# Kernel optimization log

Hardware: AMD Instinct MI355X
Metric: run time of the kernel (lower is better)

The kernel has to match this reference:

```python
import jax, jax.numpy as jnp
import numpy as np

S = 7          # number of slots
B = 8192       # batch
D = 1024       # input_dim
E = 256        # slot_embedding_dim
H = 512        # rnn_hidden_dim
SH = 256       # slot_hidden_dim
V = 100        # labels per slot (uniform)


def _lstm_cell(x, h, c, W_ih, W_hh, b_ih, b_hh):
    # PyTorch LSTMCell: gates ordered i, f, g, o
    gates = x @ W_ih.T + b_ih + h @ W_hh.T + b_hh
    i, f, g, o = jnp.split(gates, 4, axis=-1)
    i = jax.nn.sigmoid(i); f = jax.nn.sigmoid(f)
    g = jnp.tanh(g); o = jax.nn.sigmoid(o)
    c_new = f * c + i * g
    h_new = o * jnp.tanh(c_new)
    return h_new, c_new


def setup_inputs() -> dict:
    key = jax.random.key(0)
    ks = jax.random.split(key, 24)
    sc = 0.05
    D0 = D + E  # layer-0 input size
    inp = {
        'inputs': jax.random.normal(ks[0], (B, D), jnp.float32),
        'labels': jax.random.randint(ks[1], (S - 1, B), 0, V),
        'start': jax.random.normal(ks[2], (E,), jnp.float32),
        'emb': jax.random.normal(ks[3], (S - 1, V, E), jnp.float32) * sc,
        # layer 0 (input size D0)
        'W_ih0': jax.random.normal(ks[4], (S, 4 * H, D0), jnp.float32) * sc,
        'W_hh0': jax.random.normal(ks[5], (S, 4 * H, H), jnp.float32) * sc,
        'b_ih0': jax.random.normal(ks[6], (S, 4 * H), jnp.float32) * sc,
        'b_hh0': jax.random.normal(ks[7], (S, 4 * H), jnp.float32) * sc,
        'hwN_W0': jax.random.normal(ks[8], (S, H, D0 + H), jnp.float32) * sc,
        'hwN_b0': jax.random.normal(ks[9], (S, H), jnp.float32) * sc,
        'hwL_W0': jax.random.normal(ks[10], (S, H, D0), jnp.float32) * sc,
        # layer 1 (input size H)
        'W_ih1': jax.random.normal(ks[11], (S, 4 * H, H), jnp.float32) * sc,
        'W_hh1': jax.random.normal(ks[12], (S, 4 * H, H), jnp.float32) * sc,
        'b_ih1': jax.random.normal(ks[13], (S, 4 * H), jnp.float32) * sc,
        'b_hh1': jax.random.normal(ks[14], (S, 4 * H), jnp.float32) * sc,
        'hwN_W1': jax.random.normal(ks[15], (S, H, H + H), jnp.float32) * sc,
        'hwN_b1': jax.random.normal(ks[16], (S, H), jnp.float32) * sc,
        'hwL_W1': jax.random.normal(ks[17], (S, H, H), jnp.float32) * sc,
        # slot hidden + classifier
        'sh_W': jax.random.normal(ks[18], (S, SH, H), jnp.float32) * sc,
        'sh_b': jax.random.normal(ks[19], (S, SH), jnp.float32) * sc,
        'pred_W': jax.random.normal(ks[20], (S, V, SH), jnp.float32) * sc,
        'pred_b': jax.random.normal(ks[21], (S, V), jnp.float32) * sc,
    }
    return inp


def reference(inputs, labels, start, emb,
              W_ih0, W_hh0, b_ih0, b_hh0, hwN_W0, hwN_b0, hwL_W0,
              W_ih1, W_hh1, b_ih1, b_hh1, hwN_W1, hwN_b1, hwL_W1,
              sh_W, sh_b, pred_W, pred_b):
    bsz = inputs.shape[0]
    cur_emb = jnp.broadcast_to(start[None, :], (bsz, E))
    h0 = jnp.zeros((bsz, H), inputs.dtype); c0 = jnp.zeros((bsz, H), inputs.dtype)
    h1 = jnp.zeros((bsz, H), inputs.dtype); c1 = jnp.zeros((bsz, H), inputs.dtype)
    logits_all = []
    for i in range(S):  # slots are a short, structurally distinct recurrence
        x = jnp.concatenate([inputs, cur_emb], axis=-1)  # [B, D+E]
        # layer 0
        h0, c0 = _lstm_cell(x, h0, c0, W_ih0[i], W_hh0[i], b_ih0[i], b_hh0[i])
        gate = jax.nn.sigmoid(jnp.concatenate([x, h0], -1) @ hwN_W0[i].T + hwN_b0[i])
        cur = gate * h0 + (1.0 - gate) * (x @ hwL_W0[i].T)
        # layer 1
        h1, c1 = _lstm_cell(cur, h1, c1, W_ih1[i], W_hh1[i], b_ih1[i], b_hh1[i])
        gate1 = jax.nn.sigmoid(jnp.concatenate([cur, h1], -1) @ hwN_W1[i].T + hwN_b1[i])
        # (highway output of last layer feeds nothing further for this slot)
        _ = gate1 * h1 + (1.0 - gate1) * (cur @ hwL_W1[i].T)
        hidden = jax.nn.relu(h1 @ sh_W[i].T + sh_b[i])     # [B, SH]
        logits_all.append(hidden @ pred_W[i].T + pred_b[i])  # [B, V]
        if i < S - 1:
            cur_emb = emb[i][labels[i]]  # teacher-forced embedding lookup
    return jnp.stack(logits_all, axis=0)  # [S, B, V]
```

## Files before the change

kernel.cpp:

```cpp
#include <hip/hip_runtime.h>

#define SLOTS 7
#define BATCH 8192

typedef __attribute__((ext_vector_type(8))) __bf16 bf16x8;
typedef __attribute__((ext_vector_type(4))) float f32x4;

__device__ __forceinline__ void gl_lds16(const __bf16* g, __bf16* l) {
  __builtin_amdgcn_global_load_lds(
      (const __attribute__((address_space(1))) void*)g,
      (__attribute__((address_space(3))) void*)l, 16, 0, 0);
}

__device__ __forceinline__ float sigmoidf_(float x) {
  return 1.f / (1.f + __expf(-x));
}
__device__ __forceinline__ float tanhf_(float x) {
  float xc = fminf(fmaxf(x, -15.f), 15.f);
  float e = __expf(2.f * xc);
  return (e - 1.f) / (e + 1.f);
}

__global__ void __launch_bounds__(256, 4)
gemm_lstm(const __bf16* __restrict__ A, int lda,
          const __bf16* __restrict__ Bw, int ldb,
          const float* __restrict__ b_ih, const float* __restrict__ b_hh,
          float* __restrict__ cst, __bf16* __restrict__ hout, int hld, int hoff,
          int K) {
  __shared__ __align__(16) __bf16 As[2][128 * 32];
  __shared__ __align__(16) __bf16 Bs[2][128 * 32];
  const int w = threadIdx.x >> 6;
  const int lane = threadIdx.x & 63;
  const int wr = w >> 1, wc = w & 1;
  const int rowBase = blockIdx.y << 7;
  const int colBase = blockIdx.x << 7;
  const int sr = lane >> 2;
  const int scs = (((lane & 3) ^ ((sr >> 1) & 3)) << 3);

  f32x4 acc[4][4];
#pragma unroll
  for (int i = 0; i < 4; ++i)
#pragma unroll
    for (int j = 0; j < 4; ++j) acc[i][j] = (f32x4){0.f, 0.f, 0.f, 0.f};

  const int nsteps = K >> 5;

#define STAGE(bi, k0)                                                            \
  {                                                                              \
    const __bf16* ga = A + (size_t)(rowBase + (w << 5) + sr) * lda + (k0) + scs; \
    gl_lds16(ga, &As[(bi)][(w << 5) * 32]);                                      \
    gl_lds16(ga + (size_t)16 * lda, &As[(bi)][((w << 5) + 16) * 32]);            \
    const __bf16* gb = Bw + (size_t)(colBase + (w << 5) + sr) * ldb + (k0) + scs;\
    gl_lds16(gb, &Bs[(bi)][(w << 5) * 32]);                                      \
    gl_lds16(gb + (size_t)16 * ldb, &Bs[(bi)][((w << 5) + 16) * 32]);            \
  }

  STAGE(0, 0);
  __syncthreads();
  int buf = 0;
  const int ln = lane & 15;
  const int lh = lane >> 4;
  const int swz = ((lh ^ ((ln >> 1) & 3)) << 3);
  for (int t = 0; t < nsteps; ++t) {
    if (t + 1 < nsteps) STAGE(buf ^ 1, (t + 1) << 5);
    bf16x8 av[4], bv[4];
#pragma unroll
    for (int i = 0; i < 4; ++i)
      av[i] = *(const bf16x8*)&As[buf][((wr << 6) + (i << 4) + ln) * 32 + swz];
#pragma unroll
    for (int i = 0; i < 4; ++i)
      bv[i] = *(const bf16x8*)&Bs[buf][((wc << 6) + (i << 4) + ln) * 32 + swz];
#pragma unroll
    for (int mi = 0; mi < 4; ++mi)
#pragma unroll
      for (int ni = 0; ni < 4; ++ni)
        acc[mi][ni] = __builtin_amdgcn_mfma_f32_16x16x32_bf16(
            av[mi], bv[ni], acc[mi][ni], 0, 0, 0);
    __syncthreads();
    buf ^= 1;
  }
#undef STAGE

  const int row0 = rowBase + (wr << 6) + (lh << 2);
  const int h = (((colBase >> 6) + wc) << 4) + ln;
  const float bs0 = b_ih[h] + b_hh[h];
  const float bs1 = b_ih[512 + h] + b_hh[512 + h];
  const float bs2 = b_ih[1024 + h] + b_hh[1024 + h];
  const float bs3 = b_ih[1536 + h] + b_hh[1536 + h];
#pragma unroll
  for (int mi = 0; mi < 4; ++mi)
#pragma unroll
    for (int r = 0; r < 4; ++r) {
      const int row = row0 + (mi << 4) + r;
      float gi = sigmoidf_(acc[mi][0][r] + bs0);
      float gf = sigmoidf_(acc[mi][1][r] + bs1);
      float gg = tanhf_(acc[mi][2][r] + bs2);
      float go = sigmoidf_(acc[mi][3][r] + bs3);
      const size_t ci = (size_t)row * 512 + h;
      float cn = gf * cst[ci] + gi * gg;
      cst[ci] = cn;
      hout[(size_t)row * hld + hoff + h] = (__bf16)(go * tanhf_(cn));
    }
}

template <int MODE>
__global__ void __launch_bounds__(256)
gemm_bt(const __bf16* __restrict__ A, int lda,
        const __bf16* __restrict__ Bw, int ldb,
        void* __restrict__ Cout, int ldc,
        const float* __restrict__ bias,
        const float* __restrict__ auxr,
        __bf16* __restrict__ hout, int hld, int hoff,
        const __bf16* __restrict__ hsrc,
        int M, int N, int K, int Nreal) {
  __shared__ __align__(16) __bf16 As[2][128 * 32];
  __shared__ __align__(16) __bf16 Bs[2][128 * 32];
  const int w = threadIdx.x >> 6;
  const int lane = threadIdx.x & 63;
  const int wr = w >> 1, wc = w & 1;
  const int rowBase = blockIdx.y << 7;
  const int colBase = blockIdx.x << 7;
  const int sr = lane >> 2;
  const int sc = (lane & 3) << 3;

  f32x4 acc[4][4];
#pragma unroll
  for (int i = 0; i < 4; ++i)
#pragma unroll
    for (int j = 0; j < 4; ++j) acc[i][j] = (f32x4){0.f, 0.f, 0.f, 0.f};

  const int nsteps = K >> 5;

#define STAGE(bi, k0)                                                           \
  {                                                                             \
    const __bf16* ga = A + (size_t)(rowBase + (w << 5) + sr) * lda + (k0) + sc; \
    gl_lds16(ga, &As[(bi)][(w << 5) * 32]);                                     \
    gl_lds16(ga + (size_t)16 * lda, &As[(bi)][((w << 5) + 16) * 32]);           \
    const __bf16* gb = Bw + (size_t)(colBase + (w << 5) + sr) * ldb + (k0) + sc;\
    gl_lds16(gb, &Bs[(bi)][(w << 5) * 32]);                                     \
    gl_lds16(gb + (size_t)16 * ldb, &Bs[(bi)][((w << 5) + 16) * 32]);           \
  }

  STAGE(0, 0);
  __syncthreads();
  int buf = 0;
  const int ln = lane & 15;
  const int kg = (lane >> 4) << 3;
  for (int t = 0; t < nsteps; ++t) {
    if (t + 1 < nsteps) STAGE(buf ^ 1, (t + 1) << 5);
    bf16x8 av[4], bv[4];
#pragma unroll
    for (int i = 0; i < 4; ++i)
      av[i] = *(const bf16x8*)&As[buf][((wr << 6) + (i << 4) + ln) * 32 + kg];
#pragma unroll
    for (int i = 0; i < 4; ++i)
      bv[i] = *(const bf16x8*)&Bs[buf][((wc << 6) + (i << 4) + ln) * 32 + kg];
#pragma unroll
    for (int mi = 0; mi < 4; ++mi)
#pragma unroll
      for (int ni = 0; ni < 4; ++ni)
        acc[mi][ni] = __builtin_amdgcn_mfma_f32_16x16x32_bf16(
            av[mi], bv[ni], acc[mi][ni], 0, 0, 0);
    __syncthreads();
    buf ^= 1;
  }
#undef STAGE

  const int lh = lane >> 4;
  const int row0 = rowBase + (wr << 6) + (lh << 2);
  const int col0 = colBase + (wc << 6) + ln;

  if (MODE == 0) {
    float* C = (float*)Cout;
#pragma unroll
    for (int mi = 0; mi < 4; ++mi)
#pragma unroll
      for (int ni = 0; ni < 4; ++ni) {
        const int col = col0 + (ni << 4);
#pragma unroll
        for (int r = 0; r < 4; ++r)
          C[(size_t)(row0 + (mi << 4) + r) * ldc + col] = acc[mi][ni][r];
      }
  } else if (MODE == 1) {
    __bf16* C = (__bf16*)Cout;
#pragma unroll
    for (int mi = 0; mi < 4; ++mi)
#pragma unroll
      for (int ni = 0; ni < 4; ++ni) {
        const int col = col0 + (ni << 4);
        const float b = bias[col];
#pragma unroll
        for (int r = 0; r < 4; ++r) {
          float v = fmaxf(acc[mi][ni][r] + b, 0.f);
          C[(size_t)(row0 + (mi << 4) + r) * ldc + col] = (__bf16)v;
        }
      }
  } else if (MODE == 2) {
    float* C = (float*)Cout;
#pragma unroll
    for (int mi = 0; mi < 4; ++mi)
#pragma unroll
      for (int ni = 0; ni < 4; ++ni) {
        const int col = col0 + (ni << 4);
        if (col < Nreal) {
          const float b = bias[col];
#pragma unroll
          for (int r = 0; r < 4; ++r)
            C[(size_t)(row0 + (mi << 4) + r) * ldc + col] = acc[mi][ni][r] + b;
        }
      }
  } else if (MODE == 6) {
    __bf16* C = (__bf16*)Cout;
#pragma unroll
    for (int mi = 0; mi < 4; ++mi)
#pragma unroll
      for (int ni = 0; ni < 4; ++ni) {
        const int col = col0 + (ni << 4);
#pragma unroll
        for (int r = 0; r < 4; ++r) {
          const int row = row0 + (mi << 4) + r;
          float xp = auxr[(size_t)row * 1024 + col];
          float hwl = auxr[(size_t)row * 1024 + 512 + col];
          float gn = sigmoidf_(acc[mi][ni][r] + xp + bias[col]);
          float hn = (float)hsrc[(size_t)row * 512 + col];
          C[(size_t)row * ldc + col] = (__bf16)(gn * hn + (1.f - gn) * hwl);
          hout[(size_t)row * hld + hoff + col] = (__bf16)hn;
        }
      }
  }
}

#define PR0 2621440
#define PR1 3670016
#define PR2 4325376
#define PR3 4980736
#define PR4 5242880
#define PR5 6291456
#define PR6 7340032
#define PR7 7471104
#define PR8 7503872
__global__ void pack_all(const float* __restrict__ W_ih0, const float* __restrict__ W_hh0,
                         const float* __restrict__ hwN_W0, const float* __restrict__ hwL_W0,
                         const float* __restrict__ W_ih1, const float* __restrict__ W_hh1,
                         const float* __restrict__ sh_W, const float* __restrict__ pred_W,
                         __bf16* __restrict__ WA, __bf16* __restrict__ WX,
                         __bf16* __restrict__ WH, __bf16* __restrict__ WB,
                         __bf16* __restrict__ WS, __bf16* __restrict__ WP, int s) {
  const int idx = blockIdx.x * 256 + threadIdx.x;
  if (idx >= PR8) return;
  if (idx < PR0) {
    int i = idx, r = i / 1280, c = i - r * 1280;
    int sr = (((r >> 4) & 3) << 9) + ((r >> 6) << 4) + (r & 15);
    WA[(long)r * 1792 + c] = (__bf16)W_ih0[(size_t)s * 2048 * 1280 + (long)sr * 1280 + c];
  } else if (idx < PR1) {
    int i = idx - PR0, r = i >> 9, c = i & 511;
    int sr = (((r >> 4) & 3) << 9) + ((r >> 6) << 4) + (r & 15);
    WA[(long)r * 1792 + 1280 + c] = (__bf16)W_hh0[(size_t)s * 2048 * 512 + (long)sr * 512 + c];
  } else if (idx < PR2) {
    int i = idx - PR1, r = i / 1280, c = i - r * 1280;
    WX[(long)r * 1280 + c] = (__bf16)hwN_W0[(size_t)s * 512 * 1792 + (long)r * 1792 + c];
  } else if (idx < PR3) {
    int i = idx - PR2, r = i / 1280, c = i - r * 1280;
    WX[(long)(512 + r) * 1280 + c] = (__bf16)hwL_W0[(size_t)s * 512 * 1280 + (long)r * 1280 + c];
  } else if (idx < PR4) {
    int i = idx - PR3, r = i >> 9, c = i & 511;
    WH[(long)r * 512 + c] = (__bf16)hwN_W0[(size_t)s * 512 * 1792 + (long)r * 1792 + 1280 + c];
  } else if (idx < PR5) {
    int i = idx - PR4, r = i >> 9, c = i & 511;
    int sr = (((r >> 4) & 3) << 9) + ((r >> 6) << 4) + (r & 15);
    WB[(long)r * 1024 + c] = (__bf16)W_ih1[(size_t)s * 2048 * 512 + (long)sr * 512 + c];
  } else if (idx < PR6) {
    int i = idx - PR5, r = i >> 9, c = i & 511;
    int sr = (((r >> 4) & 3) << 9) + ((r >> 6) << 4) + (r & 15);
    WB[(long)r * 1024 + 512 + c] = (__bf16)W_hh1[(size_t)s * 2048 * 512 + (long)sr * 512 + c];
  } else if (idx < PR7) {
    int i = idx - PR6, r = i >> 9, c = i & 511;
    WS[(long)r * 512 + c] = (__bf16)sh_W[(size_t)s * 256 * 512 + (long)r * 512 + c];
  } else {
    int i = idx - PR7, r = i >> 8, c = i & 255;
    float v = (r < 100) ? pred_W[(size_t)s * 100 * 256 + (long)r * 256 + c] : 0.f;
    WP[(long)r * 256 + c] = (__bf16)v;
  }
}

__global__ void conv_inputs(const float* __restrict__ in, __bf16* __restrict__ xh) {
  int idx = blockIdx.x * 256 + threadIdx.x;
  int b = idx >> 10, c = idx & 1023;
  xh[(size_t)b * 1792 + c] = (__bf16)in[idx];
}

__global__ void set_start(const float* __restrict__ start, __bf16* __restrict__ xh) {
  int idx = blockIdx.x * 256 + threadIdx.x;
  int b = idx >> 8, e = idx & 255;
  xh[(size_t)b * 1792 + 1024 + e] = (__bf16)start[e];
}

__global__ void emb_gather(const float* __restrict__ emb, const int* __restrict__ labels,
                           __bf16* __restrict__ xh) {
  int idx = blockIdx.x * 256 + threadIdx.x;
  int b = idx >> 8, e = idx & 255;
  int lab = labels[b];
  xh[(size_t)b * 1792 + 1024 + e] = (__bf16)emb[(size_t)lab * 256 + e];
}

__global__ void zero_states(__bf16* __restrict__ xh, __bf16* __restrict__ xh1A) {
  int idx = blockIdx.x * 256 + threadIdx.x;
  int b = idx >> 9, h = idx & 511;
  xh[(size_t)b * 1792 + 1280 + h] = (__bf16)0.f;
  xh1A[(size_t)b * 1024 + 512 + h] = (__bf16)0.f;
}

extern "C" void kernel_launch(void* const* d_in, const int* in_sizes, int n_in,
                              void* d_out, int out_size, void* d_ws, size_t ws_size,
                              hipStream_t stream) {
  const float* inputs = (const float*)d_in[0];
  const int* labels = (const int*)d_in[1];
  const float* start = (const float*)d_in[2];
  const float* emb = (const float*)d_in[3];
  const float* W_ih0 = (const float*)d_in[4];
  const float* W_hh0 = (const float*)d_in[5];
  const float* b_ih0 = (const float*)d_in[6];
  const float* b_hh0 = (const float*)d_in[7];
  const float* hwN_W0 = (const float*)d_in[8];
  const float* hwN_b0 = (const float*)d_in[9];
  const float* hwL_W0 = (const float*)d_in[10];
  const float* W_ih1 = (const float*)d_in[11];
  const float* W_hh1 = (const float*)d_in[12];
  const float* b_ih1 = (const float*)d_in[13];
  const float* b_hh1 = (const float*)d_in[14];
  const float* sh_W = (const float*)d_in[18];
  const float* sh_b = (const float*)d_in[19];
  const float* pred_W = (const float*)d_in[20];
  const float* pred_b = (const float*)d_in[21];
  float* out = (float*)d_out;

  char* p = (char*)d_ws;
  size_t off = 0;
  auto alloc = [&](size_t bytes) {
    void* r = p + off;
    off += (bytes + 255) & ~(size_t)255;
    return r;
  };
  __bf16* WA = (__bf16*)alloc((size_t)2048 * 1792 * 2);
  __bf16* WX = (__bf16*)alloc((size_t)1024 * 1280 * 2);
  __bf16* WH = (__bf16*)alloc((size_t)512 * 512 * 2);
  __bf16* WB = (__bf16*)alloc((size_t)2048 * 1024 * 2);
  __bf16* WS = (__bf16*)alloc((size_t)256 * 512 * 2);
  __bf16* WP = (__bf16*)alloc((size_t)128 * 256 * 2);
  __bf16* xh = (__bf16*)alloc((size_t)BATCH * 1792 * 2);
  __bf16* xh1A = (__bf16*)alloc((size_t)BATCH * 1024 * 2);
  __bf16* xh1B = (__bf16*)alloc((size_t)BATCH * 1024 * 2);
  __bf16* h0new = (__bf16*)alloc((size_t)BATCH * 512 * 2);
  float* ghw = (float*)alloc((size_t)BATCH * 1024 * 4);
  float* c0 = (float*)alloc((size_t)BATCH * 512 * 4);
  float* c1 = (float*)alloc((size_t)BATCH * 512 * 4);
  __bf16* hidden = (__bf16*)ghw;
  (void)ws_size; (void)in_sizes; (void)n_in; (void)out_size;

  hipMemsetAsync(c0, 0, (size_t)BATCH * 512 * 4, stream);
  hipMemsetAsync(c1, 0, (size_t)BATCH * 512 * 4, stream);
  zero_states<<<BATCH * 512 / 256, 256, 0, stream>>>(xh, xh1A);
  conv_inputs<<<BATCH * 1024 / 256, 256, 0, stream>>>(inputs, xh);
  set_start<<<BATCH * 256 / 256, 256, 0, stream>>>(start, xh);

  const dim3 blk(256);
  for (int s = 0; s < SLOTS; ++s) {
    __bf16* xcur = (s & 1) ? xh1B : xh1A;
    __bf16* xnext = (s & 1) ? xh1A : xh1B;
    pack_all<<<(PR8 + 255) / 256, blk, 0, stream>>>(
        W_ih0, W_hh0, hwN_W0, hwL_W0, W_ih1, W_hh1, sh_W, pred_W,
        WA, WX, WH, WB, WS, WP, s);

    gemm_bt<0><<<dim3(8, 64), blk, 0, stream>>>(
        xh, 1792, WX, 1280, ghw, 1024, nullptr,
        nullptr, nullptr, 0, 0, nullptr, BATCH, 1024, 1280, 1024);
    gemm_lstm<<<dim3(16, 64), blk, 0, stream>>>(
        xh, 1792, WA, 1792, b_ih0 + s * 2048, b_hh0 + s * 2048,
        c0, h0new, 512, 0, 1792);
    gemm_bt<6><<<dim3(4, 64), blk, 0, stream>>>(
        h0new, 512, WH, 512, xcur, 1024, hwN_b0 + s * 512,
        ghw, xh, 1792, 1280, h0new, BATCH, 512, 512, 512);
    if (s < SLOTS - 1)
      emb_gather<<<BATCH * 256 / 256, blk, 0, stream>>>(
          emb + (size_t)s * 100 * 256, labels + (size_t)s * BATCH, xh);
    gemm_lstm<<<dim3(16, 64), blk, 0, stream>>>(
        xcur, 1024, WB, 1024, b_ih1 + s * 2048, b_hh1 + s * 2048,
        c1, xnext, 1024, 512, 1024);
    gemm_bt<1><<<dim3(2, 64), blk, 0, stream>>>(
        xnext + 512, 1024, WS, 512, hidden, 256, sh_b + s * 256,
        nullptr, nullptr, 0, 0, nullptr, BATCH, 256, 512, 256);
    gemm_bt<2><<<dim3(1, 64), blk, 0, stream>>>(
        hidden, 256, WP, 256, out + (size_t)s * BATCH * 100, 100,
        pred_b + s * 100, nullptr, nullptr, 0, 0, nullptr, BATCH, 128, 256, 100);
  }
}
```

Measured before the change: 1.695 ms.

## Remap blocks across XCDs, store highway preactivations in bf16, fuse embedding gather

Adds an XCD-aware block index remap to both GEMM kernels so consecutive tiles land on the same chiplet, which should improve L2 reuse. The intermediate buffer holding x-projections for the highway gate and linear path is stored in bf16 instead of fp32, halving its write and read traffic. The per-slot embedding gather kernel is removed and folded into the MODE 6 highway epilogue, saving a launch. The bf16 intermediate adds rounding error to the gate and linear terms, and the remap assumes the block count is divisible by 8.

New measurement: 1.584 ms. -6.6%, faster.

```diff
diff --git a/kernel.cpp b/kernel.cpp
--- a/kernel.cpp
+++ b/kernel.cpp
@@ -19,6 +19,15 @@
   float xc = fminf(fmaxf(x, -15.f), 15.f);
   float e = __expf(2.f * xc);
   return (e - 1.f) / (e + 1.f);
+}
+
+__device__ __forceinline__ void xcd_remap(int& bx, int& by) {
+  const int NBx = gridDim.x;
+  const int NB = NBx * gridDim.y;
+  int id = by * NBx + bx;
+  id = (id & 7) * (NB >> 3) + (id >> 3);
+  bx = id % NBx;
+  by = id / NBx;
 }
 
 __global__ void __launch_bounds__(256, 4)
@@ -32,8 +41,10 @@
   const int w = threadIdx.x >> 6;
   const int lane = threadIdx.x & 63;
   const int wr = w >> 1, wc = w & 1;
-  const int rowBase = blockIdx.y << 7;
-  const int colBase = blockIdx.x << 7;
+  int bx = blockIdx.x, by = blockIdx.y;
+  xcd_remap(bx, by);
+  const int rowBase = by << 7;
+  const int colBase = bx << 7;
   const int sr = lane >> 2;
   const int scs = (((lane & 3) ^ ((sr >> 1) & 3)) << 3);
 
@@ -109,17 +120,20 @@
         const __bf16* __restrict__ Bw, int ldb,
         void* __restrict__ Cout, int ldc,
         const float* __restrict__ bias,
-        const float* __restrict__ auxr,
+        const __bf16* __restrict__ auxr,
         __bf16* __restrict__ hout, int hld, int hoff,
         const __bf16* __restrict__ hsrc,
+        const float* __restrict__ embp, const int* __restrict__ labels, int do_emb,
         int M, int N, int K, int Nreal) {
   __shared__ __align__(16) __bf16 As[2][128 * 32];
   __shared__ __align__(16) __bf16 Bs[2][128 * 32];
   const int w = threadIdx.x >> 6;
   const int lane = threadIdx.x & 63;
   const int wr = w >> 1, wc = w & 1;
-  const int rowBase = blockIdx.y << 7;
-  const int colBase = blockIdx.x << 7;
+  int bx = blockIdx.x, by = blockIdx.y;
+  xcd_remap(bx, by);
+  const int rowBase = by << 7;
+  const int colBase = bx << 7;
   const int sr = lane >> 2;
   const int sc = (lane & 3) << 3;
 
@@ -170,18 +184,7 @@
   const int row0 = rowBase + (wr << 6) + (lh << 2);
   const int col0 = colBase + (wc << 6) + ln;
 
-  if (MODE == 0) {
-    float* C = (float*)Cout;
-#pragma unroll
-    for (int mi = 0; mi < 4; ++mi)
-#pragma unroll
-      for (int ni = 0; ni < 4; ++ni) {
-        const int col = col0 + (ni << 4);
-#pragma unroll
-        for (int r = 0; r < 4; ++r)
-          C[(size_t)(row0 + (mi << 4) + r) * ldc + col] = acc[mi][ni][r];
-      }
-  } else if (MODE == 1) {
+  if (MODE == 1) {
     __bf16* C = (__bf16*)Cout;
 #pragma unroll
     for (int mi = 0; mi < 4; ++mi)
@@ -209,6 +212,17 @@
             C[(size_t)(row0 + (mi << 4) + r) * ldc + col] = acc[mi][ni][r] + b;
         }
       }
+  } else if (MODE == 7) {
+    __bf16* C = (__bf16*)Cout;
+#pragma unroll
+    for (int mi = 0; mi < 4; ++mi)
+#pragma unroll
+      for (int ni = 0; ni < 4; ++ni) {
+        const int col = col0 + (ni << 4);
+#pragma unroll
+        for (int r = 0; r < 4; ++r)
+          C[(size_t)(row0 + (mi << 4) + r) * ldc + col] = (__bf16)acc[mi][ni][r];
+      }
   } else if (MODE == 6) {
     __bf16* C = (__bf16*)Cout;
 #pragma unroll
@@ -219,14 +233,29 @@
 #pragma unroll
         for (int r = 0; r < 4; ++r) {
           const int row = row0 + (mi << 4) + r;
-          float xp = auxr[(size_t)row * 1024 + col];
-          float hwl = auxr[(size_t)row * 1024 + 512 + col];
+          float xp = (float)auxr[(size_t)row * 1024 + col];
+          float hwl = (float)auxr[(size_t)row * 1024 + 512 + col];
           float gn = sigmoidf_(acc[mi][ni][r] + xp + bias[col]);
           float hn = (float)hsrc[(size_t)row * 512 + col];
           C[(size_t)row * ldc + col] = (__bf16)(gn * hn + (1.f - gn) * hwl);
           hout[(size_t)row * hld + hoff + col] = (__bf16)hn;
         }
       }
+    if (do_emb && colBase < 256) {
+#pragma unroll
+      for (int mi = 0; mi < 4; ++mi)
+#pragma unroll
+        for (int r = 0; r < 4; ++r) {
+          const int row = row0 + (mi << 4) + r;
+          const int lab = labels[row];
+#pragma unroll
+          for (int ni = 0; ni < 4; ++ni) {
+            const int col = col0 + (ni << 4);
+            hout[(size_t)row * hld + 1024 + col] =
+                (__bf16)embp[(size_t)lab * 256 + col];
+          }
+        }
+    }
   }
 }
 
@@ -295,14 +324,6 @@
   xh[(size_t)b * 1792 + 1024 + e] = (__bf16)start[e];
 }
 
-__global__ void emb_gather(const float* __restrict__ emb, const int* __restrict__ labels,
-                           __bf16* __restrict__ xh) {
-  int idx = blockIdx.x * 256 + threadIdx.x;
-  int b = idx >> 8, e = idx & 255;
-  int lab = labels[b];
-  xh[(size_t)b * 1792 + 1024 + e] = (__bf16)emb[(size_t)lab * 256 + e];
-}
-
 __global__ void zero_states(__bf16* __restrict__ xh, __bf16* __restrict__ xh1A) {
   int idx = blockIdx.x * 256 + threadIdx.x;
   int b = idx >> 9, h = idx & 511;
@@ -351,7 +372,7 @@
   __bf16* xh1A = (__bf16*)alloc((size_t)BATCH * 1024 * 2);
   __bf16* xh1B = (__bf16*)alloc((size_t)BATCH * 1024 * 2);
   __bf16* h0new = (__bf16*)alloc((size_t)BATCH * 512 * 2);
-  float* ghw = (float*)alloc((size_t)BATCH * 1024 * 4);
+  __bf16* ghw = (__bf16*)alloc((size_t)BATCH * 1024 * 2);
   float* c0 = (float*)alloc((size_t)BATCH * 512 * 4);
   float* c1 = (float*)alloc((size_t)BATCH * 512 * 4);
   __bf16* hidden = (__bf16*)ghw;
@@ -371,26 +392,28 @@
         W_ih0, W_hh0, hwN_W0, hwL_W0, W_ih1, W_hh1, sh_W, pred_W,
         WA, WX, WH, WB, WS, WP, s);
 
-    gemm_bt<0><<<dim3(8, 64), blk, 0, stream>>>(
+    gemm_bt<7><<<dim3(8, 64), blk, 0, stream>>>(
         xh, 1792, WX, 1280, ghw, 1024, nullptr,
-        nullptr, nullptr, 0, 0, nullptr, BATCH, 1024, 1280, 1024);
+        nullptr, nullptr, 0, 0, nullptr, nullptr, nullptr, 0,
+        BATCH, 1024, 1280, 1024);
     gemm_lstm<<<dim3(16, 64), blk, 0, stream>>>(
         xh, 1792, WA, 1792, b_ih0 + s * 2048, b_hh0 + s * 2048,
         c0, h0new, 512, 0, 1792);
     gemm_bt<6><<<dim3(4, 64), blk, 0, stream>>>(
         h0new, 512, WH, 512, xcur, 1024, hwN_b0 + s * 512,
-        ghw, xh, 1792, 1280, h0new, BATCH, 512, 512, 512);
-    if (s < SLOTS - 1)
-      emb_gather<<<BATCH * 256 / 256, blk, 0, stream>>>(
-          emb + (size_t)s * 100 * 256, labels + (size_t)s * BATCH, xh);
+        ghw, xh, 1792, 1280, h0new,
+        emb + (size_t)s * 100 * 256, labels + (size_t)s * BATCH,
+        (s < SLOTS - 1) ? 1 : 0, BATCH, 512, 512, 512);
     gemm_lstm<<<dim3(16, 64), blk, 0, stream>>>(
         xcur, 1024, WB, 1024, b_ih1 + s * 2048, b_hh1 + s * 2048,
         c1, xnext, 1024, 512, 1024);
     gemm_bt<1><<<dim3(2, 64), blk, 0, stream>>>(
         xnext + 512, 1024, WS, 512, hidden, 256, sh_b + s * 256,
-        nullptr, nullptr, 0, 0, nullptr, BATCH, 256, 512, 256);
+        nullptr, nullptr, 0, 0, nullptr, nullptr, nullptr, 0,
+        BATCH, 256, 512, 256);
     gemm_bt<2><<<dim3(1, 64), blk, 0, stream>>>(
         hidden, 256, WP, 256, out + (size_t)s * BATCH * 100, 100,
-        pred_b + s * 100, nullptr, nullptr, 0, 0, nullptr, BATCH, 128, 256, 100);
-  }
-}
+        pred_b + s * 100, nullptr, nullptr, 0, 0, nullptr, nullptr, nullptr, 0,
+        BATCH, 128, 256, 100);
+  }
+}
```
